# Performance work log

Hardware: AMD Instinct MI355X
Metric: run time of the kernel (lower is better)

## Reference

```python
import jax, jax.numpy as jnp
import numpy as np

EMBED_DIM = 512
Q_DIM = 64
V_DIM = 64
WINDOW_SIZE = 128
B, N = 2, 4096


def setup_inputs() -> dict:
    key = jax.random.key(0)
    ks = jax.random.split(key, 7)
    s = 1.0 / np.sqrt(EMBED_DIM)
    u = lambda k, shape: jax.random.uniform(k, shape, jnp.float32, -s, s)
    return {
        "x": jax.random.normal(ks[0], (B, N, EMBED_DIM), jnp.float32),
        "Wq": u(ks[1], (EMBED_DIM, Q_DIM)),
        "bq": u(ks[2], (Q_DIM,)),
        "Wk": u(ks[3], (EMBED_DIM, Q_DIM)),
        "bk": u(ks[4], (Q_DIM,)),
        "Wv": u(ks[5], (EMBED_DIM, V_DIM)),
        "bv": u(ks[6], (V_DIM,)),
    }


def reference(x, Wq, bq, Wk, bk, Wv, bv):
    b, n, _ = x.shape
    w = WINDOW_SIZE // 2
    Q = x @ Wq + bq  # (b, n, Qd)
    K = x @ Wk + bk  # (b, n, Qd)
    V = x @ Wv + bv  # (b, n, Vd)

    diags = jnp.arange(-w, w + 1)            # (nd,) offsets di
    nd = diags.shape[0]
    # Gather K[i + di] via padded K; invalid positions masked to 0 afterwards.
    Kpad = jnp.pad(K, ((0, 0), (w, w), (0, 0)))
    j = jnp.arange(n)[:, None] + diags[None, :]          # (n, nd) = i + di
    Kg = Kpad[:, j + w, :]                               # (b, n, nd, Qd)
    scores = jnp.einsum('bnd,bnod->bno', Q, Kg)          # (b, n, nd)
    valid = (j >= 0) & (j < n)
    scores = jnp.where(valid[None], scores, 0.0)

    # Faithful to original: diagonal dot products are scattered into the FIRST
    # nd columns of a dense (b, n, n) matrix (rest zeros), softmax over the
    # full n columns, then dense matmul with V.
    columns = jnp.zeros((b, n, n), dtype=x.dtype).at[:, :, :nd].set(scores)
    attn = jax.nn.softmax(columns, axis=2)               # (b, n, n)
    return attn @ V                                      # (b, n, Vd)
```

## Files before the change

kernel.cpp:

```cpp
#include <hip/hip_runtime.h>

typedef _Float16 half8 __attribute__((ext_vector_type(8)));
typedef float f32x4 __attribute__((ext_vector_type(4)));

#define NN 4096
#define NE 512
#define HD 64
#define KROWS 4288
#define KOFF  64
#define WSCALE (1.0f / 256.0f)

__device__ __forceinline__ void f16_split(float f, _Float16& hi, _Float16& lo) {
    hi = (_Float16)f;
    lo = (_Float16)(f - (float)hi);
}

#define MFMA16(a, b, c) __builtin_amdgcn_mfma_f32_16x16x32_f16((a), (b), (c), 0, 0, 0)

__global__ __launch_bounds__(256) void wprep_kernel(
    const float* __restrict__ Wq, const float* __restrict__ Wk,
    const float* __restrict__ Wv,
    _Float16* __restrict__ Wf, _Float16* __restrict__ Khi,
    _Float16* __restrict__ Vf, float* __restrict__ Vs)
{
    const int gtid = blockIdx.x * 256 + threadIdx.x;
    const int L = gtid & 63;
    {
        const int nt = (gtid >> 6) % 12;
        const int kt = gtid / 768;
        const int n = nt * 16 + (L & 15);
        const int kbase = kt * 32 + (L >> 4) * 8;
        const float* src; int col;
        if (n < 64)       { src = Wq; col = n; }
        else if (n < 128) { src = Wk; col = n - 64; }
        else              { src = Wv; col = n - 128; }
        half8 sh;
#pragma unroll
        for (int j = 0; j < 8; ++j)
            sh[j] = (_Float16)src[(size_t)(kbase + j) * HD + col];
        *(half8*)(Wf + (size_t)gtid * 8) = sh;
    }
    if (gtid < 6144) {
        const int p = gtid >> 3, o = gtid & 7;
        const int b = p / 192, q = p - b * 192;
        const size_t row = (size_t)b * KROWS + (q < 64 ? q : 4096 + q);
        const half8 z = {0, 0, 0, 0, 0, 0, 0, 0};
        *(half8*)(Khi + row * HD + o * 8) = z;
    }
    if (gtid < 3200) {
        const int rem = gtid % 1600;
        const int jt = rem / 320;
        const int nt = (rem / 64) % 5;
        half8 sh = {0, 0, 0, 0, 0, 0, 0, 0};
        if (nt == 4 && (L & 15) == 0) {
#pragma unroll
            for (int jj = 0; jj < 8; ++jj) {
                const int j = jt * 32 + (L >> 4) * 8 + jj;
                if (j < 129) sh[jj] = (_Float16)1.0f;
            }
        }
        *(half8*)(Vf + (size_t)gtid * 8) = sh;
    }
    if (gtid < 128) Vs[gtid] = 0.f;
}

__global__ __launch_bounds__(512) void proj_kernel(
    const float* __restrict__ x, const _Float16* __restrict__ Wf,
    const float* __restrict__ bq, const float* __restrict__ bk,
    const float* __restrict__ bv,
    _Float16* __restrict__ Qhi, _Float16* __restrict__ Qlo,
    _Float16* __restrict__ Khi, _Float16* __restrict__ Vf,
    float* __restrict__ Vs)
{
    __shared__ float parts[4][3][64][4];
    __shared__ float V_lds[16][68];
    const int tid = threadIdx.x;
    const int L = tid & 63;
    const int w = tid >> 6;
    const int m = L & 15, kg = L >> 4;
    const int blk = blockIdx.x;
    const int r0 = blk * 16;
    const int b = blk >> 8;
    const int t3 = w & 3;
    const int h = w >> 2;

    const float* xp = x + (size_t)(r0 + m) * NE + h * 256 + kg * 8;
    const _Float16* wfb = Wf + ((size_t)(h * 8) * 12 + t3 * 3) * 512 + L * 8;

    f32x4 acc[3];
#pragma unroll
    for (int t = 0; t < 3; ++t) acc[t] = (f32x4){0.f, 0.f, 0.f, 0.f};

#pragma unroll
    for (int kt = 0; kt < 8; ++kt) {
        const float4 x0 = *(const float4*)(xp + kt * 32);
        const float4 x1 = *(const float4*)(xp + kt * 32 + 4);
        const float xv[8] = {x0.x, x0.y, x0.z, x0.w, x1.x, x1.y, x1.z, x1.w};
        half8 ahi, alo;
#pragma unroll
        for (int j = 0; j < 8; ++j) {
            _Float16 hh, ll; f16_split(xv[j], hh, ll);
            ahi[j] = hh; alo[j] = ll;
        }
#pragma unroll
        for (int t = 0; t < 3; ++t) {
            const half8 wv = *(const half8*)(wfb + (size_t)kt * 6144 + t * 512);
            acc[t] = MFMA16(ahi, wv, acc[t]);
            acc[t] = MFMA16(alo, wv, acc[t]);
        }
    }

    if (h == 1) {
#pragma unroll
        for (int t = 0; t < 3; ++t)
            *(f32x4*)(&parts[t3][t][L][0]) = acc[t];
    }
    __syncthreads();

    if (h == 0) {
#pragma unroll
        for (int t = 0; t < 3; ++t) {
            const f32x4 p = *(const f32x4*)(&parts[t3][t][L][0]);
            acc[t] += p;
            const int nt = t3 * 3 + t;
            const int cgc = nt * 16 + m;
            const float bias = (cgc < 64) ? bq[cgc]
                             : (cgc < 128) ? bk[cgc - 64] : bv[cgc - 128];
#pragma unroll
            for (int r = 0; r < 4; ++r) {
                const int gr = r0 + kg * 4 + r;
                const float val = acc[t][r] + bias;
                if (cgc < 64) {
                    _Float16 hh, ll; f16_split(val, hh, ll);
                    Qhi[(size_t)gr * HD + cgc] = hh;
                    Qlo[(size_t)gr * HD + cgc] = ll;
                } else if (cgc < 128) {
                    const int d = cgc - 64, n = gr & 4095;
                    Khi[((size_t)b * KROWS + KOFF + n) * HD + d] = (_Float16)val;
                } else {
                    V_lds[kg * 4 + r][cgc - 128] = val;
                }
            }
        }
    }
    __syncthreads();

    if (tid < 64) {
        float s = 0.f;
#pragma unroll
        for (int r = 0; r < 16; ++r) s += V_lds[r][tid];
        atomicAdd(&Vs[b * HD + tid], s);
    }

    {
        const int local = blk & 255;
        if (local < 8 && w < 4) {
            const int jt = local >> 1;
            if ((kg >> 1) == (local & 1)) {
                const int nt = w;
                half8 sh;
#pragma unroll
                for (int jj = 0; jj < 8; ++jj) {
                    const int lrow = (kg - (local & 1) * 2) * 8 + jj;
                    sh[jj] = (_Float16)V_lds[lrow][nt * 16 + m];
                }
                const size_t fo = ((size_t)((b * 25 + jt * 5 + nt) * 64 + L)) * 8;
                *(half8*)(Vf + fo) = sh;
            }
        } else if (local == 8 && w < 4 && kg == 0) {
            const int nt = w;
            half8 sh = {0, 0, 0, 0, 0, 0, 0, 0};
            sh[0] = (_Float16)V_lds[0][nt * 16 + m];
            const size_t fo = ((size_t)((b * 25 + 4 * 5 + nt) * 64 + L)) * 8;
            *(half8*)(Vf + fo) = sh;
        }
    }
}

__global__ __launch_bounds__(256) void attn_kernel(
    const _Float16* __restrict__ Qhi, const _Float16* __restrict__ Qlo,
    const _Float16* __restrict__ Khi, const _Float16* __restrict__ Vf,
    const float* __restrict__ Vs, float* __restrict__ out)
{
    __shared__ __align__(16) _Float16 wt_hi[16 * 168];
    __shared__ __align__(16) _Float16 wt_lo[16 * 168];
    __shared__ float den_lds[16];

    const int tid = threadIdx.x;
    const int L = tid & 63;
    const int w = tid >> 6;
    const int m = L & 15, kg = L >> 4;
    const int b = blockIdx.x >> 8;
    const int n0 = (blockIdx.x & 255) * 16;

    const _Float16* qp  = Qhi + ((size_t)(b * NN + n0 + m)) * HD + kg * 8;
    const _Float16* qp2 = Qlo + ((size_t)(b * NN + n0 + m)) * HD + kg * 8;
    const half8 qhi0 = *(const half8*)(qp);
    const half8 qhi1 = *(const half8*)(qp + 32);
    const half8 qlo0 = *(const half8*)(qp2);
    const half8 qlo1 = *(const half8*)(qp2 + 32);

    int kts[3]; int nkt;
    if (w == 3) { kts[0] = 3; kts[1] = 7; kts[2] = 8; nkt = 3; }
    else        { kts[0] = w; kts[1] = w + 4; kts[2] = 0; nkt = 2; }

    const _Float16* KB = Khi + (size_t)b * KROWS * HD;
    half8 kh0[3], kh1[3];
#pragma unroll
    for (int i = 0; i < 3; ++i) {
        if (i < nkt) {
            const _Float16* kp = KB + (size_t)(n0 + kts[i] * 16 + m) * HD + kg * 8;
            kh0[i] = *(const half8*)(kp);
            kh1[i] = *(const half8*)(kp + 32);
        }
    }

    half8 vhi[5], vh4[5];
#pragma unroll
    for (int jt = 0; jt < 5; ++jt) {
        const size_t fo = ((size_t)((b * 25 + jt * 5 + w) * 64 + L)) * 8;
        vhi[jt] = *(const half8*)(Vf + fo);
    }
    if (w == 0) {
#pragma unroll
        for (int jt = 0; jt < 5; ++jt) {
            const size_t fo4 = ((size_t)((b * 25 + jt * 5 + 4) * 64 + L)) * 8;
            vh4[jt] = *(const half8*)(Vf + fo4);
        }
    }

    for (int i = tid; i < (16 * 168) / 2; i += 256) {
        ((int*)wt_hi)[i] = 0;
        ((int*)wt_lo)[i] = 0;
    }
    __syncthreads();

#pragma unroll
    for (int i = 0; i < 3; ++i) {
        if (i < nkt) {
            f32x4 acc = (f32x4){0.f, 0.f, 0.f, 0.f};
            acc = MFMA16(qhi0, kh0[i], acc);
            acc = MFMA16(qhi1, kh1[i], acc);
            acc = MFMA16(qlo0, kh0[i], acc);
            acc = MFMA16(qlo1, kh1[i], acc);
            const int l = kts[i] * 16 + m;
#pragma unroll
            for (int r = 0; r < 4; ++r) {
                const int q = kg * 4 + r;
                const int j = l - q;
                if (j >= 0 && j < 129) {
                    const float wval = (__expf(acc[r]) - 1.0f) * WSCALE;
                    _Float16 hh, ll; f16_split(wval, hh, ll);
                    wt_hi[q * 168 + j] = hh;
                    wt_lo[q * 168 + j] = ll;
                }
            }
        }
    }
    __syncthreads();

    f32x4 oacc = (f32x4){0.f, 0.f, 0.f, 0.f};
    f32x4 dacc = (f32x4){0.f, 0.f, 0.f, 0.f};
#pragma unroll
    for (int jt = 0; jt < 5; ++jt) {
        const half8 whi = *(const half8*)(wt_hi + m * 168 + jt * 32 + kg * 8);
        const half8 wlo = *(const half8*)(wt_lo + m * 168 + jt * 32 + kg * 8);
        oacc = MFMA16(whi, vhi[jt], oacc);
        oacc = MFMA16(wlo, vhi[jt], oacc);
        if (w == 0) {
            dacc = MFMA16(whi, vh4[jt], dacc);
            dacc = MFMA16(wlo, vh4[jt], dacc);
        }
    }
    if (w == 0 && m == 0) {
#pragma unroll
        for (int r = 0; r < 4; ++r) den_lds[kg * 4 + r] = dacc[r];
    }
    __syncthreads();

    {
        const float vs = Vs[b * HD + w * 16 + m];
#pragma unroll
        for (int r = 0; r < 4; ++r) {
            const int q = kg * 4 + r;
            const float val = (vs + 256.0f * oacc[r])
                            / (4096.f + 256.0f * den_lds[q]);
            out[((size_t)(b * NN + n0 + q)) * HD + w * 16 + m] = val;
        }
    }
}

extern "C" void kernel_launch(void* const* d_in, const int* in_sizes, int n_in,
                              void* d_out, int out_size, void* d_ws, size_t ws_size,
                              hipStream_t stream)
{
    const float* x  = (const float*)d_in[0];
    const float* Wq = (const float*)d_in[1];
    const float* bq = (const float*)d_in[2];
    const float* Wk = (const float*)d_in[3];
    const float* bk = (const float*)d_in[4];
    const float* Wv = (const float*)d_in[5];
    const float* bv = (const float*)d_in[6];
    float* out = (float*)d_out;

    char* ws = (char*)d_ws;
    float*     Vs  = (float*)(ws + 0);
    _Float16*  Khi = (_Float16*)(ws + 512);
    _Float16*  Qhi = (_Float16*)(ws + 1098240);
    _Float16*  Qlo = (_Float16*)(ws + 2146816);
    _Float16*  Wf  = (_Float16*)(ws + 3195392);
    _Float16*  Vf  = (_Float16*)(ws + 3392000);

    wprep_kernel<<<48, 256, 0, stream>>>(Wq, Wk, Wv, Wf, Khi, Vf, Vs);
    proj_kernel<<<512, 512, 0, stream>>>(x, Wf, bq, bk, bv,
                                         Qhi, Qlo, Khi, Vf, Vs);
    attn_kernel<<<512, 256, 0, stream>>>(Qhi, Qlo, Khi, Vf, Vs, out);
}
```

Measured before the change: 98.07 us.

## Pre-split x into fp16 hi/lo fragment layout in prep kernel; simplify projection

The weight-prep kernel now also converts x into fp16 hi/lo halves stored in MFMA-fragment order in workspace. The projection kernel drops to 256 threads with each wave covering the full K range, which removes the LDS split-K reduction and a barrier. This costs an extra full pass over x: fp32 is read once and 16 MB of fp16 is written, then read back by the projection. The projection in turn gets contiguous fragment loads and no conversion work.

New measurement: 99.43 us. Within noise of the previous version (+1.4%).

```diff
diff --git a/kernel.cpp b/kernel.cpp
--- a/kernel.cpp
+++ b/kernel.cpp
@@ -17,62 +17,90 @@
 
 #define MFMA16(a, b, c) __builtin_amdgcn_mfma_f32_16x16x32_f16((a), (b), (c), 0, 0, 0)
 
-__global__ __launch_bounds__(256) void wprep_kernel(
+__global__ __launch_bounds__(256) void prep_kernel(
+    const float* __restrict__ x,
     const float* __restrict__ Wq, const float* __restrict__ Wk,
     const float* __restrict__ Wv,
     _Float16* __restrict__ Wf, _Float16* __restrict__ Khi,
-    _Float16* __restrict__ Vf, float* __restrict__ Vs)
+    _Float16* __restrict__ Vf, float* __restrict__ Vs,
+    _Float16* __restrict__ Xfhi, _Float16* __restrict__ Xflo)
 {
-    const int gtid = blockIdx.x * 256 + threadIdx.x;
-    const int L = gtid & 63;
-    {
-        const int nt = (gtid >> 6) % 12;
-        const int kt = gtid / 768;
-        const int n = nt * 16 + (L & 15);
-        const int kbase = kt * 32 + (L >> 4) * 8;
-        const float* src; int col;
-        if (n < 64)       { src = Wq; col = n; }
-        else if (n < 128) { src = Wk; col = n - 64; }
-        else              { src = Wv; col = n - 128; }
-        half8 sh;
-#pragma unroll
-        for (int j = 0; j < 8; ++j)
-            sh[j] = (_Float16)src[(size_t)(kbase + j) * HD + col];
-        *(half8*)(Wf + (size_t)gtid * 8) = sh;
-    }
-    if (gtid < 6144) {
-        const int p = gtid >> 3, o = gtid & 7;
-        const int b = p / 192, q = p - b * 192;
-        const size_t row = (size_t)b * KROWS + (q < 64 ? q : 4096 + q);
-        const half8 z = {0, 0, 0, 0, 0, 0, 0, 0};
-        *(half8*)(Khi + row * HD + o * 8) = z;
-    }
-    if (gtid < 3200) {
-        const int rem = gtid % 1600;
-        const int jt = rem / 320;
-        const int nt = (rem / 64) % 5;
-        half8 sh = {0, 0, 0, 0, 0, 0, 0, 0};
-        if (nt == 4 && (L & 15) == 0) {
-#pragma unroll
-            for (int jj = 0; jj < 8; ++jj) {
-                const int j = jt * 32 + (L >> 4) * 8 + jj;
-                if (j < 129) sh[jj] = (_Float16)1.0f;
-            }
-        }
-        *(half8*)(Vf + (size_t)gtid * 8) = sh;
-    }
-    if (gtid < 128) Vs[gtid] = 0.f;
-}
-
-__global__ __launch_bounds__(512) void proj_kernel(
-    const float* __restrict__ x, const _Float16* __restrict__ Wf,
+    const int blk = blockIdx.x;
+    if (blk < 48) {
+        const int gtid = blk * 256 + threadIdx.x;
+        const int L = gtid & 63;
+        {
+            const int nt = (gtid >> 6) % 12;
+            const int kt = gtid / 768;
+            const int n = nt * 16 + (L & 15);
+            const int kbase = kt * 32 + (L >> 4) * 8;
+            const float* src; int col;
+            if (n < 64)       { src = Wq; col = n; }
+            else if (n < 128) { src = Wk; col = n - 64; }
+            else              { src = Wv; col = n - 128; }
+            half8 sh;
+#pragma unroll
+            for (int j = 0; j < 8; ++j)
+                sh[j] = (_Float16)src[(size_t)(kbase + j) * HD + col];
+            *(half8*)(Wf + (size_t)gtid * 8) = sh;
+        }
+        if (gtid < 6144) {
+            const int p = gtid >> 3, o = gtid & 7;
+            const int b = p / 192, q = p - b * 192;
+            const size_t row = (size_t)b * KROWS + (q < 64 ? q : 4096 + q);
+            const half8 z = {0, 0, 0, 0, 0, 0, 0, 0};
+            *(half8*)(Khi + row * HD + o * 8) = z;
+        }
+        if (gtid < 3200) {
+            const int rem = gtid % 1600;
+            const int jt = rem / 320;
+            const int nt = (rem / 64) % 5;
+            half8 sh = {0, 0, 0, 0, 0, 0, 0, 0};
+            if (nt == 4 && (L & 15) == 0) {
+#pragma unroll
+                for (int jj = 0; jj < 8; ++jj) {
+                    const int j = jt * 32 + (L >> 4) * 8 + jj;
+                    if (j < 129) sh[jj] = (_Float16)1.0f;
+                }
+            }
+            *(half8*)(Vf + (size_t)gtid * 8) = sh;
+        }
+        if (gtid < 128) Vs[gtid] = 0.f;
+    } else {
+        const int gt = (blk - 48) * 256 + threadIdx.x;
+#pragma unroll
+        for (int i = 0; i < 4; ++i) {
+            const int s = gt + i * 131072;
+            const int rt = s >> 10;
+            const int kt = (s >> 6) & 15;
+            const int L = s & 63;
+            const int row = rt * 16 + (L & 15);
+            const int k = kt * 32 + (L >> 4) * 8;
+            const float4 x0 = *(const float4*)(x + (size_t)row * NE + k);
+            const float4 x1 = *(const float4*)(x + (size_t)row * NE + k + 4);
+            const float xv[8] = {x0.x, x0.y, x0.z, x0.w,
+                                 x1.x, x1.y, x1.z, x1.w};
+            half8 hh, ll;
+#pragma unroll
+            for (int j = 0; j < 8; ++j) {
+                _Float16 h, l; f16_split(xv[j], h, l);
+                hh[j] = h; ll[j] = l;
+            }
+            *(half8*)(Xfhi + (size_t)s * 8) = hh;
+            *(half8*)(Xflo + (size_t)s * 8) = ll;
+        }
+    }
+}
+
+__global__ __launch_bounds__(256) void proj_kernel(
+    const _Float16* __restrict__ Xfhi, const _Float16* __restrict__ Xflo,
+    const _Float16* __restrict__ Wf,
     const float* __restrict__ bq, const float* __restrict__ bk,
     const float* __restrict__ bv,
     _Float16* __restrict__ Qhi, _Float16* __restrict__ Qlo,
     _Float16* __restrict__ Khi, _Float16* __restrict__ Vf,
     float* __restrict__ Vs)
 {
-    __shared__ float parts[4][3][64][4];
     __shared__ float V_lds[16][68];
     const int tid = threadIdx.x;
     const int L = tid & 63;
@@ -81,65 +109,46 @@
     const int blk = blockIdx.x;
     const int r0 = blk * 16;
     const int b = blk >> 8;
-    const int t3 = w & 3;
-    const int h = w >> 2;
-
-    const float* xp = x + (size_t)(r0 + m) * NE + h * 256 + kg * 8;
-    const _Float16* wfb = Wf + ((size_t)(h * 8) * 12 + t3 * 3) * 512 + L * 8;
 
     f32x4 acc[3];
 #pragma unroll
     for (int t = 0; t < 3; ++t) acc[t] = (f32x4){0.f, 0.f, 0.f, 0.f};
 
-#pragma unroll
-    for (int kt = 0; kt < 8; ++kt) {
-        const float4 x0 = *(const float4*)(xp + kt * 32);
-        const float4 x1 = *(const float4*)(xp + kt * 32 + 4);
-        const float xv[8] = {x0.x, x0.y, x0.z, x0.w, x1.x, x1.y, x1.z, x1.w};
-        half8 ahi, alo;
-#pragma unroll
-        for (int j = 0; j < 8; ++j) {
-            _Float16 hh, ll; f16_split(xv[j], hh, ll);
-            ahi[j] = hh; alo[j] = ll;
-        }
+    const _Float16* xf = Xfhi + ((size_t)blk * 16 * 64 + L) * 8;
+    const _Float16* xl = Xflo + ((size_t)blk * 16 * 64 + L) * 8;
+    const _Float16* wf = Wf + ((size_t)(w * 3) * 64 + L) * 8;
+
+#pragma unroll
+    for (int kt = 0; kt < 16; ++kt) {
+        const half8 ahi = *(const half8*)(xf + (size_t)kt * 512);
+        const half8 alo = *(const half8*)(xl + (size_t)kt * 512);
 #pragma unroll
         for (int t = 0; t < 3; ++t) {
-            const half8 wv = *(const half8*)(wfb + (size_t)kt * 6144 + t * 512);
+            const half8 wv = *(const half8*)(wf + ((size_t)kt * 12 + t) * 512);
             acc[t] = MFMA16(ahi, wv, acc[t]);
             acc[t] = MFMA16(alo, wv, acc[t]);
         }
     }
 
-    if (h == 1) {
-#pragma unroll
-        for (int t = 0; t < 3; ++t)
-            *(f32x4*)(&parts[t3][t][L][0]) = acc[t];
-    }
-    __syncthreads();
-
-    if (h == 0) {
-#pragma unroll
-        for (int t = 0; t < 3; ++t) {
-            const f32x4 p = *(const f32x4*)(&parts[t3][t][L][0]);
-            acc[t] += p;
-            const int nt = t3 * 3 + t;
-            const int cgc = nt * 16 + m;
-            const float bias = (cgc < 64) ? bq[cgc]
-                             : (cgc < 128) ? bk[cgc - 64] : bv[cgc - 128];
-#pragma unroll
-            for (int r = 0; r < 4; ++r) {
-                const int gr = r0 + kg * 4 + r;
-                const float val = acc[t][r] + bias;
-                if (cgc < 64) {
-                    _Float16 hh, ll; f16_split(val, hh, ll);
-                    Qhi[(size_t)gr * HD + cgc] = hh;
-                    Qlo[(size_t)gr * HD + cgc] = ll;
-                } else if (cgc < 128) {
-                    const int d = cgc - 64, n = gr & 4095;
-                    Khi[((size_t)b * KROWS + KOFF + n) * HD + d] = (_Float16)val;
-                } else {
-                    V_lds[kg * 4 + r][cgc - 128] = val;
-                }
+#pragma unroll
+    for (int t = 0; t < 3; ++t) {
+        const int nt = w * 3 + t;
+        const int cgc = nt * 16 + m;
+        const float bias = (cgc < 64) ? bq[cgc]
+                         : (cgc < 128) ? bk[cgc - 64] : bv[cgc - 128];
+#pragma unroll
+        for (int r = 0; r < 4; ++r) {
+            const int gr = r0 + kg * 4 + r;
+            const float val = acc[t][r] + bias;
+            if (cgc < 64) {
+                _Float16 hh, ll; f16_split(val, hh, ll);
+                Qhi[(size_t)gr * HD + cgc] = hh;
+                Qlo[(size_t)gr * HD + cgc] = ll;
+            } else if (cgc < 128) {
+                const int d = cgc - 64, n = gr & 4095;
+                Khi[((size_t)b * KROWS + KOFF + n) * HD + d] = (_Float16)val;
+            } else {
+                V_lds[kg * 4 + r][cgc - 128] = val;
             }
         }
     }
@@ -154,7 +163,7 @@
 
     {
         const int local = blk & 255;
-        if (local < 8 && w < 4) {
+        if (local < 8) {
             const int jt = local >> 1;
             if ((kg >> 1) == (local & 1)) {
                 const int nt = w;
@@ -167,7 +176,7 @@
                 const size_t fo = ((size_t)((b * 25 + jt * 5 + nt) * 64 + L)) * 8;
                 *(half8*)(Vf + fo) = sh;
             }
-        } else if (local == 8 && w < 4 && kg == 0) {
+        } else if (local == 8 && kg == 0) {
             const int nt = w;
             half8 sh = {0, 0, 0, 0, 0, 0, 0, 0};
             sh[0] = (_Float16)V_lds[0][nt * 16 + m];
@@ -304,15 +313,18 @@
     float* out = (float*)d_out;
 
     char* ws = (char*)d_ws;
-    float*     Vs  = (float*)(ws + 0);
-    _Float16*  Khi = (_Float16*)(ws + 512);
-    _Float16*  Qhi = (_Float16*)(ws + 1098240);
-    _Float16*  Qlo = (_Float16*)(ws + 2146816);
-    _Float16*  Wf  = (_Float16*)(ws + 3195392);
-    _Float16*  Vf  = (_Float16*)(ws + 3392000);
-
-    wprep_kernel<<<48, 256, 0, stream>>>(Wq, Wk, Wv, Wf, Khi, Vf, Vs);
-    proj_kernel<<<512, 512, 0, stream>>>(x, Wf, bq, bk, bv,
+    float*     Vs   = (float*)(ws + 0);
+    _Float16*  Khi  = (_Float16*)(ws + 512);
+    _Float16*  Qhi  = (_Float16*)(ws + 1098240);
+    _Float16*  Qlo  = (_Float16*)(ws + 2146816);
+    _Float16*  Wf   = (_Float16*)(ws + 3195392);
+    _Float16*  Vf   = (_Float16*)(ws + 3392000);
+    _Float16*  Xfhi = (_Float16*)(ws + 3443200);
+    _Float16*  Xflo = (_Float16*)(ws + 11831808);
+
+    prep_kernel<<<560, 256, 0, stream>>>(x, Wq, Wk, Wv, Wf, Khi, Vf, Vs,
+                                         Xfhi, Xflo);
+    proj_kernel<<<512, 256, 0, stream>>>(Xfhi, Xflo, Wf, bq, bk, bv,
                                          Qhi, Qlo, Khi, Vf, Vs);
     attn_kernel<<<512, 256, 0, stream>>>(Qhi, Qlo, Khi, Vf, Vs, out);
 }
```
